# Performance work log

Hardware: AMD Instinct MI355X
Metric: run time of the kernel (lower is better)

## Reference

```python
import jax, jax.numpy as jnp
import numpy as np

N, F_IN, HID, OUT, H = 10000, 256, 256, 512, 4
E = 320000
SLOPE = 0.2  # GATv2Conv default negative_slope
EPS = 1e-5   # LayerNorm eps


def setup_inputs() -> dict:
    key = jax.random.key(0)
    ks = jax.random.split(key, 10)
    g = lambda k, shape, fan: (jax.random.normal(k, shape, jnp.float32) / np.float32(np.sqrt(fan)))
    d1, d2 = HID // H, OUT // H
    return {
        "x": jax.random.normal(ks[0], (N, F_IN), jnp.float32),
        "edge_index": jax.random.randint(ks[1], (2, E), 0, N),
        # layer 1 (in_feats -> hidden_dim, heads=H, concat)
        "Wl1": g(ks[2], (HID, F_IN), F_IN), "bl1": jnp.zeros((HID,), jnp.float32),
        "Wr1": g(ks[3], (HID, F_IN), F_IN), "br1": jnp.zeros((HID,), jnp.float32),
        "att1": g(ks[4], (H, d1), d1), "bias1": jnp.zeros((HID,), jnp.float32),
        # layer 2 (hidden_dim -> out_dim)
        "Wl2": g(ks[5], (OUT, HID), HID), "bl2": jnp.zeros((OUT,), jnp.float32),
        "Wr2": g(ks[6], (OUT, HID), HID), "br2": jnp.zeros((OUT,), jnp.float32),
        "att2": g(ks[7], (H, d2), d2), "bias2": jnp.zeros((OUT,), jnp.float32),
        # final LayerNorm
        "gamma": jnp.ones((OUT,), jnp.float32), "beta": jnp.zeros((OUT,), jnp.float32),
    }


def _gatv2(x, src, dst, Wl, bl, Wr, br, att, bias, heads):
    """GATv2Conv: e_ij = a_h . leaky_relu(Wl x_j + Wr x_i), softmax over j per i,
    out_i = sum_j alpha_ij * (Wl x_j), heads concatenated, plus bias."""
    n = x.shape[0]
    d = Wl.shape[0] // heads
    xl = (x @ Wl.T + bl).reshape(n, heads, d)  # source transform
    xr = (x @ Wr.T + br).reshape(n, heads, d)  # target transform
    s = jax.nn.leaky_relu(xl[src] + xr[dst], SLOPE)        # [E,H,d]
    e = jnp.einsum('ehd,hd->eh', s, att)                   # [E,H]
    m = jax.ops.segment_max(e, dst, num_segments=n)        # [N,H] (self-loops => no empty segs)
    w = jnp.exp(e - m[dst])
    denom = jax.ops.segment_sum(w, dst, num_segments=n)
    alpha = w / denom[dst]                                 # segment softmax
    out = jax.ops.segment_sum(alpha[:, :, None] * xl[src], dst, num_segments=n)  # [N,H,d]
    return out.reshape(n, heads * d) + bias


def reference(x, edge_index, Wl1, bl1, Wr1, br1, att1, bias1,
              Wl2, bl2, Wr2, br2, att2, bias2, gamma, beta):
    n = x.shape[0]
    loop = jnp.arange(n, dtype=edge_index.dtype)  # add_self_loops=True
    src = jnp.concatenate([edge_index[0], loop])
    dst = jnp.concatenate([edge_index[1], loop])
    h = jax.nn.relu(_gatv2(x, src, dst, Wl1, bl1, Wr1, br1, att1, bias1, H))
    h = _gatv2(h, src, dst, Wl2, bl2, Wr2, br2, att2, bias2, H)
    mu = jnp.mean(h, axis=-1, keepdims=True)
    var = jnp.var(h, axis=-1, keepdims=True)
    return gamma * (h - mu) / jnp.sqrt(var + EPS) + beta
```

## Files before the change

### kernel.cpp

```cpp
#include <hip/hip_runtime.h>
#include <stdint.h>

#define N_NODES 10000
#define K_DIM   256
#define HID_D   256
#define OUT_D   512
#define NE      320000
#define NE_TOT  (NE + N_NODES)
#define SLOPE   0.2f
#define LN_EPS  1e-5f

typedef __bf16 bf16x8 __attribute__((ext_vector_type(8)));
typedef float  f32x4  __attribute__((ext_vector_type(4)));
typedef unsigned short u16;
typedef uint32_t u32;

__device__ __forceinline__ float bf2f(u16 u) {
    union { u32 i; float f; } v; v.i = ((u32)u) << 16; return v.f;
}
__device__ __forceinline__ u16 f2bf(float f) {
    union { float f; u32 i; } v; v.f = f;
    u32 b = v.i;
    return (u16)((b + 0x7FFFu + ((b >> 16) & 1u)) >> 16);
}
__device__ __forceinline__ void bf2x2(u32 u, float& lo, float& hi) {
    union { u32 i; float f; } a, b;
    a.i = u << 16; b.i = u & 0xFFFF0000u;
    lo = a.f; hi = b.f;
}
__device__ __forceinline__ u32 pack2bf(float a, float b) {
    return (u32)f2bf(a) | ((u32)f2bf(b) << 16);
}

__global__ __launch_bounds__(256) void k_detect(const u32* __restrict__ x,
                                                int* __restrict__ flag) {
    u32 v = x[threadIdx.x];
    int e_lo = (int)((v >> 7) & 0xFF);
    int vote = (e_lo >= 100 && e_lo <= 150) ? 1 : 0;
    __shared__ int cnt;
    if (threadIdx.x == 0) cnt = 0;
    __syncthreads();
    atomicAdd(&cnt, vote);
    __syncthreads();
    if (threadIdx.x == 0) *flag = (cnt > 180) ? 1 : 0;
}

struct CanonW {
    const void *x, *wl1, *wr1, *wl2, *wr2;
    u16 *xd, *wl1d, *wr1d, *wl2d, *wr2d;
};
#define CW_X  2560000
#define CW_1  (CW_X + 65536)
#define CW_2  (CW_1 + 65536)
#define CW_3  (CW_2 + 131072)
#define CW_TOT (CW_3 + 131072)
__global__ __launch_bounds__(256) void k_canon_w(CanonW c, const int* __restrict__ flag) {
    int i = blockIdx.x * 256 + threadIdx.x;
    const void* src; u16* dst; int off;
    if      (i < CW_X) { src = c.x;   dst = c.xd;   off = i; }
    else if (i < CW_1) { src = c.wl1; dst = c.wl1d; off = i - CW_X; }
    else if (i < CW_2) { src = c.wr1; dst = c.wr1d; off = i - CW_1; }
    else if (i < CW_3) { src = c.wl2; dst = c.wl2d; off = i - CW_2; }
    else               { src = c.wr2; dst = c.wr2d; off = i - CW_3; }
    if (*flag) dst[off] = ((const u16*)src)[off];
    else       dst[off] = f2bf(((const float*)src)[off]);
}

struct CanonS { const void* src[10]; float* dst[10]; };
__global__ __launch_bounds__(256) void k_canon_s(CanonS c, const int* __restrict__ flag) {
    int i = blockIdx.x * 256 + threadIdx.x;
    int seg, off;
    if (i < 1024) { seg = i >> 8; off = i & 255; }
    else          { seg = 4 + ((i - 1024) >> 9); off = (i - 1024) & 511; }
    const void* s = c.src[seg];
    float* d = c.dst[seg];
    d[off] = (*flag) ? bf2f(((const u16*)s)[off]) : ((const float*)s)[off];
}


__global__ __launch_bounds__(256) void k_init_deg(int* deg) {
    int i = blockIdx.x * 256 + threadIdx.x;
    if (i < N_NODES) deg[i] = 1;
}

__global__ __launch_bounds__(256) void k_count_deg(const int* __restrict__ ei, int* deg) {
    int e = blockIdx.x * 256 + threadIdx.x;
    if (e < NE) atomicAdd(&deg[ei[NE + e]], 1);
}

__global__ __launch_bounds__(1024) void k_scan(const int* __restrict__ deg,
                                               int* __restrict__ rowptr,
                                               int* __restrict__ cursor) {
    __shared__ int sbuf[2][1024];
    int t = threadIdx.x;
    int base = t * 10;
    int loc[10];
    int s = 0;
    #pragma unroll
    for (int q = 0; q < 10; ++q) {
        int idx = base + q;
        int d = (idx < N_NODES) ? deg[idx] : 0;
        loc[q] = s;
        s += d;
    }
    sbuf[0][t] = s;
    __syncthreads();
    int cur = 0;
    for (int off = 1; off < 1024; off <<= 1) {
        int nxt = cur ^ 1;
        int v = sbuf[cur][t];
        if (t >= off) v += sbuf[cur][t - off];
        sbuf[nxt][t] = v;
        __syncthreads();
        cur = nxt;
    }
    int excl = sbuf[cur][t] - s;
    #pragma unroll
    for (int q = 0; q < 10; ++q) {
        int idx = base + q;
        if (idx <= N_NODES) {
            int val = excl + loc[q];
            rowptr[idx] = val;
            cursor[idx] = val;
        }
    }
}

__global__ __launch_bounds__(256) void k_scatter(const int* __restrict__ ei,
                                                 int* cursor, int* __restrict__ csr_src) {
    int e = blockIdx.x * 256 + threadIdx.x;
    if (e >= NE_TOT) return;
    int s, d;
    if (e < NE) { s = ei[e]; d = ei[NE + e]; }
    else        { s = e - NE; d = s; }
    int pos = atomicAdd(&cursor[d], 1);
    csr_src[pos] = s;
}

__global__ __launch_bounds__(256) void k_gemm2(const u16* __restrict__ X,
                                               const u16* __restrict__ Wl,
                                               const u16* __restrict__ Wr,
                                               const float* __restrict__ bl,
                                               const float* __restrict__ br,
                                               u16* __restrict__ Yl,
                                               u16* __restrict__ Yr, int Ncols) {
    int nb = Ncols >> 6;
    int by = blockIdx.y;
    const u16* W; const float* bias; u16* Y; int nbase;
    if (by < nb) { W = Wl; bias = bl; Y = Yl; nbase = by * 64; }
    else         { W = Wr; bias = br; Y = Yr; nbase = (by - nb) * 64; }

    int m0   = blockIdx.x * 64;
    int wave = threadIdx.x >> 6;
    int lane = threadIdx.x & 63;
    int quad = lane >> 4;
    int l16  = lane & 15;
    int n0   = nbase + wave * 16;

    const u16* wrow = W + (size_t)(n0 + l16) * K_DIM + quad * 8;
    const u16* arow[4];
    #pragma unroll
    for (int r = 0; r < 4; ++r) {
        int row = m0 + r * 16 + l16;
        if (row >= N_NODES) row = N_NODES - 1;
        arow[r] = X + (size_t)row * K_DIM + quad * 8;
    }

    f32x4 acc[4] = {};
    #pragma unroll
    for (int k0 = 0; k0 < K_DIM; k0 += 32) {
        bf16x8 b = *reinterpret_cast<const bf16x8*>(wrow + k0);
        #pragma unroll
        for (int r = 0; r < 4; ++r) {
            bf16x8 a = *reinterpret_cast<const bf16x8*>(arow[r] + k0);
            acc[r] = __builtin_amdgcn_mfma_f32_16x16x32_bf16(a, b, acc[r], 0, 0, 0);
        }
    }
    int col = n0 + l16;
    float bv = bias[col];
    #pragma unroll
    for (int r = 0; r < 4; ++r) {
        int rbase = m0 + r * 16 + quad * 4;
        #pragma unroll
        for (int q = 0; q < 4; ++q) {
            int row = rbase + q;
            if (row < N_NODES)
                Y[(size_t)row * Ncols + col] = f2bf(acc[r][q] + bv);
        }
    }
}

__global__ __launch_bounds__(256) void k_agg1(const u16* __restrict__ xl,
                                              const u16* __restrict__ xr,
                                              const int* __restrict__ rowptr,
                                              const int* __restrict__ csr_src,
                                              const float* __restrict__ att,
                                              const float* __restrict__ bias,
                                              u16* __restrict__ hout) {
    int wave = threadIdx.x >> 6, lane = threadIdx.x & 63;
    int i = blockIdx.x * 4 + wave;
    if (i >= N_NODES) return;
    int c0 = (lane >> 4) * 64 + (lane & 15) * 4;

    const u32* xr32 = (const u32*)(xr + (size_t)i * HID_D + c0);
    u32 xp0 = xr32[0], xp1 = xr32[1];
    float xr0, xr1v, xr2v, xr3;
    bf2x2(xp0, xr0, xr1v); bf2x2(xp1, xr2v, xr3);
    float a0 = att[c0], a1 = att[c0 + 1], a2 = att[c0 + 2], a3 = att[c0 + 3];

    int beg = rowptr[i], end = rowptr[i + 1];
    float denom = 0.f;
    float acc0 = 0.f, acc1 = 0.f, acc2 = 0.f, acc3 = 0.f;
    const u16* xbase = xl + c0;

    auto edge = [&](u32 q0, u32 q1) {
        float v0, v1, v2, v3;
        bf2x2(q0, v0, v1); bf2x2(q1, v2, v3);
        float s0 = v0 + xr0;  s0 = fmaxf(s0, s0 * SLOPE);
        float s1 = v1 + xr1v; s1 = fmaxf(s1, s1 * SLOPE);
        float s2 = v2 + xr2v; s2 = fmaxf(s2, s2 * SLOPE);
        float s3 = v3 + xr3;  s3 = fmaxf(s3, s3 * SLOPE);
        float pr = s0 * a0;
        pr = fmaf(s1, a1, pr); pr = fmaf(s2, a2, pr); pr = fmaf(s3, a3, pr);
        #pragma unroll
        for (int o = 1; o < 16; o <<= 1) pr += __shfl_xor(pr, o, 64);
        float w = __expf(fminf(pr, 60.f));
        denom += w;
        acc0 = fmaf(w, v0, acc0);
        acc1 = fmaf(w, v1, acc1);
        acc2 = fmaf(w, v2, acc2);
        acc3 = fmaf(w, v3, acc3);
    };

    for (int chunk = beg; chunk < end; chunk += 64) {
        int cnt = end - chunk; if (cnt > 64) cnt = 64;
        int myj = csr_src[chunk + ((lane < cnt) ? lane : (cnt - 1))];
        int e = 0;
        for (; e + 4 <= cnt; e += 4) {
            int j0 = __shfl(myj, e,     64);
            int j1 = __shfl(myj, e + 1, 64);
            int j2 = __shfl(myj, e + 2, 64);
            int j3 = __shfl(myj, e + 3, 64);
            const u32* r0 = (const u32*)(xbase + (size_t)j0 * HID_D);
            const u32* r1 = (const u32*)(xbase + (size_t)j1 * HID_D);
            const u32* r2 = (const u32*)(xbase + (size_t)j2 * HID_D);
            const u32* r3 = (const u32*)(xbase + (size_t)j3 * HID_D);
            u32 p00 = r0[0], p01 = r0[1];
            u32 p10 = r1[0], p11 = r1[1];
            u32 p20 = r2[0], p21 = r2[1];
            u32 p30 = r3[0], p31 = r3[1];
            edge(p00, p01); edge(p10, p11); edge(p20, p21); edge(p30, p31);
        }
        for (; e < cnt; ++e) {
            int j = __shfl(myj, e, 64);
            const u32* r = (const u32*)(xbase + (size_t)j * HID_D);
            edge(r[0], r[1]);
        }
    }

    float inv = 1.f / denom;
    float o0 = fmaxf(fmaf(acc0, inv, bias[c0]),     0.f);
    float o1 = fmaxf(fmaf(acc1, inv, bias[c0 + 1]), 0.f);
    float o2 = fmaxf(fmaf(acc2, inv, bias[c0 + 2]), 0.f);
    float o3 = fmaxf(fmaf(acc3, inv, bias[c0 + 3]), 0.f);
    u32* hp = (u32*)(hout + (size_t)i * HID_D + c0);
    hp[0] = pack2bf(o0, o1);
    hp[1] = pack2bf(o2, o3);
}

__global__ __launch_bounds__(256) void k_agg2_ln(const u16* __restrict__ xl,
                                                 const u16* __restrict__ xr,
                                                 const int* __restrict__ rowptr,
                                                 const int* __restrict__ csr_src,
                                                 const float* __restrict__ att,
                                                 const float* __restrict__ bias,
                                                 const float* __restrict__ gamma,
                                                 const float* __restrict__ beta,
                                                 void* __restrict__ outv,
                                                 const int* __restrict__ flag) {
    int wave = threadIdx.x >> 6, lane = threadIdx.x & 63;
    int i = blockIdx.x * 4 + wave;
    if (i >= N_NODES) return;
    int c0 = (lane >> 4) * 128 + (lane & 15) * 8;

    float xrv[8], a[8];
    {
        uint4 xq = *(const uint4*)(xr + (size_t)i * OUT_D + c0);
        bf2x2(xq.x, xrv[0], xrv[1]); bf2x2(xq.y, xrv[2], xrv[3]);
        bf2x2(xq.z, xrv[4], xrv[5]); bf2x2(xq.w, xrv[6], xrv[7]);
        #pragma unroll
        for (int k = 0; k < 8; ++k) a[k] = att[c0 + k];
    }

    int beg = rowptr[i], end = rowptr[i + 1];
    float denom = 0.f;
    float acc[8] = {};
    const u16* xbase = xl + c0;

    auto edge = [&](uint4 q) {
        float v[8];
        bf2x2(q.x, v[0], v[1]); bf2x2(q.y, v[2], v[3]);
        bf2x2(q.z, v[4], v[5]); bf2x2(q.w, v[6], v[7]);
        float pr = 0.f;
        #pragma unroll
        for (int k = 0; k < 8; ++k) {
            float s = v[k] + xrv[k];
            s = fmaxf(s, s * SLOPE);
            pr = fmaf(s, a[k], pr);
        }
        #pragma unroll
        for (int o = 1; o < 16; o <<= 1) pr += __shfl_xor(pr, o, 64);
        float w = __expf(fminf(pr, 60.f));
        denom += w;
        #pragma unroll
        for (int k = 0; k < 8; ++k) acc[k] = fmaf(w, v[k], acc[k]);
    };

    for (int chunk = beg; chunk < end; chunk += 64) {
        int cnt = end - chunk; if (cnt > 64) cnt = 64;
        int myj = csr_src[chunk + ((lane < cnt) ? lane : (cnt - 1))];
        int e = 0;
        for (; e + 4 <= cnt; e += 4) {
            int j0 = __shfl(myj, e,     64);
            int j1 = __shfl(myj, e + 1, 64);
            int j2 = __shfl(myj, e + 2, 64);
            int j3 = __shfl(myj, e + 3, 64);
            uint4 q0 = *(const uint4*)(xbase + (size_t)j0 * OUT_D);
            uint4 q1 = *(const uint4*)(xbase + (size_t)j1 * OUT_D);
            uint4 q2 = *(const uint4*)(xbase + (size_t)j2 * OUT_D);
            uint4 q3 = *(const uint4*)(xbase + (size_t)j3 * OUT_D);
            edge(q0); edge(q1); edge(q2); edge(q3);
        }
        for (; e < cnt; ++e) {
            int j = __shfl(myj, e, 64);
            edge(*(const uint4*)(xbase + (size_t)j * OUT_D));
        }
    }

    float inv = 1.f / denom;
    float o[8];
    float s1 = 0.f, s2 = 0.f;
    #pragma unroll
    for (int k = 0; k < 8; ++k) {
        o[k] = fmaf(acc[k], inv, bias[c0 + k]);
        s1 += o[k];
        s2 = fmaf(o[k], o[k], s2);
    }
    #pragma unroll
    for (int off = 1; off < 64; off <<= 1) {
        s1 += __shfl_xor(s1, off, 64);
        s2 += __shfl_xor(s2, off, 64);
    }
    float mu  = s1 * (1.f / OUT_D);
    float var = s2 * (1.f / OUT_D) - mu * mu;
    float rstd = rsqrtf(var + LN_EPS);

    size_t ob = (size_t)i * OUT_D + c0;
    if (*flag) {
        u32 pk[4];
        #pragma unroll
        for (int k = 0; k < 4; ++k) {
            float r0 = fmaf(gamma[c0 + 2*k]     * (o[2*k]     - mu), rstd, beta[c0 + 2*k]);
            float r1 = fmaf(gamma[c0 + 2*k + 1] * (o[2*k + 1] - mu), rstd, beta[c0 + 2*k + 1]);
            pk[k] = pack2bf(r0, r1);
        }
        *(uint4*)((u16*)outv + ob) = make_uint4(pk[0], pk[1], pk[2], pk[3]);
    } else {
        float* out = (float*)outv + ob;
        #pragma unroll
        for (int k = 0; k < 8; ++k)
            out[k] = fmaf(gamma[c0 + k] * (o[k] - mu), rstd, beta[c0 + k]);
    }
}


extern "C" void kernel_launch(void* const* d_in, const int* in_sizes, int n_in,
                              void* d_out, int out_size, void* d_ws, size_t ws_size,
                              hipStream_t stream) {
    const int* ei = (const int*)d_in[1];

    char* ws = (char*)d_ws;
    size_t off = 0;
    auto alloc = [&](size_t bytes) { void* p = ws + off; off += (bytes + 255) & ~(size_t)255; return p; };
    u16* xcb  = (u16*)alloc((size_t)N_NODES * K_DIM * 2);
    u16* wl1b = (u16*)alloc((size_t)HID_D * K_DIM * 2);
    u16* wr1b = (u16*)alloc((size_t)HID_D * K_DIM * 2);
    u16* wl2b = (u16*)alloc((size_t)OUT_D * K_DIM * 2);
    u16* wr2b = (u16*)alloc((size_t)OUT_D * K_DIM * 2);
    u16* xl1b = (u16*)alloc((size_t)N_NODES * HID_D * 2);
    u16* xr1b = (u16*)alloc((size_t)N_NODES * HID_D * 2);
    u16* hb   = (u16*)alloc((size_t)N_NODES * HID_D * 2);
    u16* xl2b = (u16*)alloc((size_t)N_NODES * OUT_D * 2);
    u16* xr2b = (u16*)alloc((size_t)N_NODES * OUT_D * 2);
    float* bl1c  = (float*)alloc(HID_D * 4);
    float* br1c  = (float*)alloc(HID_D * 4);
    float* att1c = (float*)alloc(HID_D * 4);
    float* bia1c = (float*)alloc(HID_D * 4);
    float* bl2c  = (float*)alloc(OUT_D * 4);
    float* br2c  = (float*)alloc(OUT_D * 4);
    float* att2c = (float*)alloc(OUT_D * 4);
    float* bia2c = (float*)alloc(OUT_D * 4);
    float* gamc  = (float*)alloc(OUT_D * 4);
    float* betc  = (float*)alloc(OUT_D * 4);
    int* flag = (int*)alloc(256);
    int* deg  = (int*)alloc((size_t)N_NODES * 4);
    int* rowp = (int*)alloc((size_t)(N_NODES + 1) * 4);
    int* curs = (int*)alloc((size_t)(N_NODES + 1) * 4);
    int* csrc = (int*)alloc((size_t)NE_TOT * 4);

    hipLaunchKernelGGL(k_detect, dim3(1), dim3(256), 0, stream, (const u32*)d_in[0], flag);

    CanonW cw = { d_in[0], d_in[2], d_in[4], d_in[8], d_in[10],
                  xcb, wl1b, wr1b, wl2b, wr2b };
    hipLaunchKernelGGL(k_canon_w, dim3(CW_TOT / 256), dim3(256), 0, stream, cw, flag);

    CanonS cs;
    cs.src[0] = d_in[3];  cs.dst[0] = bl1c;
    cs.src[1] = d_in[5];  cs.dst[1] = br1c;
    cs.src[2] = d_in[6];  cs.dst[2] = att1c;
    cs.src[3] = d_in[7];  cs.dst[3] = bia1c;
    cs.src[4] = d_in[9];  cs.dst[4] = bl2c;
    cs.src[5] = d_in[11]; cs.dst[5] = br2c;
    cs.src[6] = d_in[12]; cs.dst[6] = att2c;
    cs.src[7] = d_in[13]; cs.dst[7] = bia2c;
    cs.src[8] = d_in[14]; cs.dst[8] = gamc;
    cs.src[9] = d_in[15]; cs.dst[9] = betc;
    hipLaunchKernelGGL(k_canon_s, dim3(16), dim3(256), 0, stream, cs, flag);

    hipLaunchKernelGGL(k_init_deg, dim3((N_NODES + 255) / 256), dim3(256), 0, stream, deg);
    hipLaunchKernelGGL(k_count_deg, dim3((NE + 255) / 256), dim3(256), 0, stream, ei, deg);
    hipLaunchKernelGGL(k_scan, dim3(1), dim3(1024), 0, stream, deg, rowp, curs);
    hipLaunchKernelGGL(k_scatter, dim3((NE_TOT + 255) / 256), dim3(256), 0, stream, ei, curs, csrc);

    const int MB = (N_NODES + 63) / 64;
    hipLaunchKernelGGL(k_gemm2, dim3(MB, 2 * HID_D / 64), dim3(256), 0, stream,
                       xcb, wl1b, wr1b, bl1c, br1c, xl1b, xr1b, HID_D);
    hipLaunchKernelGGL(k_agg1, dim3((N_NODES + 3) / 4), dim3(256), 0, stream,
                       xl1b, xr1b, rowp, csrc, att1c, bia1c, hb);
    hipLaunchKernelGGL(k_gemm2, dim3(MB, 2 * OUT_D / 64), dim3(256), 0, stream,
                       hb, wl2b, wr2b, bl2c, br2c, xl2b, xr2b, OUT_D);
    hipLaunchKernelGGL(k_agg2_ln, dim3((N_NODES + 3) / 4), dim3(256), 0, stream,
                       xl2b, xr2b, rowp, csrc, att2c, bia2c, gamc, betc, d_out, flag);
}
```

Measured before the change: 320.6 us.

## Tile GEMM through LDS with 128x128 blocks and direct global-to-LDS loads

Rewrites the dual-projection GEMM to stage 128x64 tiles of X and W in shared memory using global_load_lds, with each wave computing a 64x64 subtile (4x4 MFMA accumulators). Previously each wave streamed its A and B fragments straight from global memory with little reuse. The change is meant to cut redundant global traffic and raise MFMA density. It adds more registers per thread, two barriers per K step with no double buffering, and fewer blocks (79x4 or 79x8), which may lower occupancy.

```diff
diff --git a/kernel.cpp b/kernel.cpp
--- a/kernel.cpp
+++ b/kernel.cpp
@@ -30,6 +30,12 @@
 }
 __device__ __forceinline__ u32 pack2bf(float a, float b) {
     return (u32)f2bf(a) | ((u32)f2bf(b) << 16);
+}
+
+__device__ __forceinline__ void gl_lds16(const u16* g, u16* lds_base) {
+    __builtin_amdgcn_global_load_lds(
+        (const __attribute__((address_space(1))) void*)g,
+        (__attribute__((address_space(3))) void*)lds_base, 16, 0, 0);
 }
 
 __global__ __launch_bounds__(256) void k_detect(const u32* __restrict__ x,
@@ -144,48 +150,76 @@
                                                const float* __restrict__ br,
                                                u16* __restrict__ Yl,
                                                u16* __restrict__ Yr, int Ncols) {
-    int nb = Ncols >> 6;
+    __shared__ uint4 sAq[1024];
+    __shared__ uint4 sBq[1024];
+    u16* sA = (u16*)sAq;
+    u16* sB = (u16*)sBq;
+
+    int nb = Ncols >> 7;
     int by = blockIdx.y;
     const u16* W; const float* bias; u16* Y; int nbase;
-    if (by < nb) { W = Wl; bias = bl; Y = Yl; nbase = by * 64; }
-    else         { W = Wr; bias = br; Y = Yr; nbase = (by - nb) * 64; }
-
-    int m0   = blockIdx.x * 64;
-    int wave = threadIdx.x >> 6;
-    int lane = threadIdx.x & 63;
+    if (by < nb) { W = Wl; bias = bl; Y = Yl; nbase = by << 7; }
+    else         { W = Wr; bias = br; Y = Yr; nbase = (by - nb) << 7; }
+
+    int m0   = blockIdx.x << 7;
+    int tid  = threadIdx.x;
+    int wave = tid >> 6;
+    int lane = tid & 63;
     int quad = lane >> 4;
     int l16  = lane & 15;
-    int n0   = nbase + wave * 16;
-
-    const u16* wrow = W + (size_t)(n0 + l16) * K_DIM + quad * 8;
-    const u16* arow[4];
+    int wm   = wave & 1;
+    int wn   = wave >> 1;
+
+    f32x4 acc[4][4] = {};
+
+    #pragma unroll 1
+    for (int kk = 0; kk < K_DIM; kk += 64) {
+        #pragma unroll
+        for (int r = 0; r < 4; ++r) {
+            int g = wave + r * 4;
+            int chunk = g >> 1;
+            int row = ((g & 1) << 6) + lane;
+            int mg = m0 + row;
+            if (mg >= N_NODES) mg = N_NODES - 1;
+            gl_lds16(X + (size_t)mg * K_DIM + kk + chunk * 8, sA + (size_t)(g << 6) * 8);
+            gl_lds16(W + (size_t)(nbase + row) * K_DIM + kk + chunk * 8, sB + (size_t)(g << 6) * 8);
+        }
+        __syncthreads();
+
+        #pragma unroll
+        for (int s = 0; s < 2; ++s) {
+            int c = s * 4 + quad;
+            bf16x8 af[4], bf[4];
+            #pragma unroll
+            for (int t = 0; t < 4; ++t) {
+                int m = (wm << 6) + t * 16 + l16;
+                af[t] = *(const bf16x8*)(sA + ((size_t)(c << 7) + m) * 8);
+                int n = (wn << 6) + t * 16 + l16;
+                bf[t] = *(const bf16x8*)(sB + ((size_t)(c << 7) + n) * 8);
+            }
+            #pragma unroll
+            for (int mt = 0; mt < 4; ++mt)
+                #pragma unroll
+                for (int nt = 0; nt < 4; ++nt)
+                    acc[mt][nt] = __builtin_amdgcn_mfma_f32_16x16x32_bf16(
+                        af[mt], bf[nt], acc[mt][nt], 0, 0, 0);
+        }
+        __syncthreads();
+    }
+
     #pragma unroll
-    for (int r = 0; r < 4; ++r) {
-        int row = m0 + r * 16 + l16;
-        if (row >= N_NODES) row = N_NODES - 1;
-        arow[r] = X + (size_t)row * K_DIM + quad * 8;
-    }
-
-    f32x4 acc[4] = {};
-    #pragma unroll
-    for (int k0 = 0; k0 < K_DIM; k0 += 32) {
-        bf16x8 b = *reinterpret_cast<const bf16x8*>(wrow + k0);
-        #pragma unroll
-        for (int r = 0; r < 4; ++r) {
-            bf16x8 a = *reinterpret_cast<const bf16x8*>(arow[r] + k0);
-            acc[r] = __builtin_amdgcn_mfma_f32_16x16x32_bf16(a, b, acc[r], 0, 0, 0);
-        }
-    }
-    int col = n0 + l16;
-    float bv = bias[col];
-    #pragma unroll
-    for (int r = 0; r < 4; ++r) {
-        int rbase = m0 + r * 16 + quad * 4;
-        #pragma unroll
-        for (int q = 0; q < 4; ++q) {
-            int row = rbase + q;
-            if (row < N_NODES)
-                Y[(size_t)row * Ncols + col] = f2bf(acc[r][q] + bv);
+    for (int nt = 0; nt < 4; ++nt) {
+        int col = nbase + (wn << 6) + nt * 16 + l16;
+        float bv = bias[col];
+        #pragma unroll
+        for (int mt = 0; mt < 4; ++mt) {
+            int rbase = m0 + (wm << 6) + mt * 16 + quad * 4;
+            #pragma unroll
+            for (int q = 0; q < 4; ++q) {
+                int row = rbase + q;
+                if (row < N_NODES)
+                    Y[(size_t)row * Ncols + col] = f2bf(acc[mt][nt][q] + bv);
+            }
         }
     }
 }
@@ -432,12 +466,12 @@
     hipLaunchKernelGGL(k_scan, dim3(1), dim3(1024), 0, stream, deg, rowp, curs);
     hipLaunchKernelGGL(k_scatter, dim3((NE_TOT + 255) / 256), dim3(256), 0, stream, ei, curs, csrc);
 
-    const int MB = (N_NODES + 63) / 64;
-    hipLaunchKernelGGL(k_gemm2, dim3(MB, 2 * HID_D / 64), dim3(256), 0, stream,
+    const int MB = (N_NODES + 127) / 128;
+    hipLaunchKernelGGL(k_gemm2, dim3(MB, 2 * HID_D / 128), dim3(256), 0, stream,
                        xcb, wl1b, wr1b, bl1c, br1c, xl1b, xr1b, HID_D);
     hipLaunchKernelGGL(k_agg1, dim3((N_NODES + 3) / 4), dim3(256), 0, stream,
                        xl1b, xr1b, rowp, csrc, att1c, bia1c, hb);
-    hipLaunchKernelGGL(k_gemm2, dim3(MB, 2 * OUT_D / 64), dim3(256), 0, stream,
+    hipLaunchKernelGGL(k_gemm2, dim3(MB, 2 * OUT_D / 128), dim3(256), 0, stream,
                        hb, wl2b, wr2b, bl2c, br2c, xl2b, xr2b, OUT_D);
     hipLaunchKernelGGL(k_agg2_ln, dim3((N_NODES + 3) / 4), dim3(256), 0, stream,
                        xl2b, xr2b, rowp, csrc, att2c, bia2c, gamc, betc, d_out, flag);
```

Result: faster. 288.6 us (-10.0%).
